# Kernel optimization log

Hardware: AMD Instinct MI355X
Metric: run time of the kernel (lower is better)

The kernel has to match this reference:

```python
import jax, jax.numpy as jnp
import numpy as np
import math

TAU = 2.0
V_TH = 1.0
DECAY = math.exp(-1.0 / TAU)  # LIF membrane decay


def setup_inputs() -> dict:
    key = jax.random.key(0)
    k_x, k_w, k_b = jax.random.split(key, 3)
    T, B, C_IN, H, W = 4, 8, 64, 128, 128
    C_OUT, K = 64, 3
    x = jax.random.normal(k_x, (T, B, C_IN, H, W), dtype=jnp.float32)
    fan_in = C_IN * K * K
    weight = jax.random.normal(k_w, (C_OUT, C_IN, K, K), dtype=jnp.float32) / jnp.sqrt(fan_in)
    bias = jax.random.normal(k_b, (C_OUT,), dtype=jnp.float32) * 0.01
    return {"x": x, "weight": weight, "bias": bias}


def reference(x, weight, bias):
    # x: [T, B, C_IN, H, W]; 3x3 conv, stride 1, pad 1 -> same spatial size
    T, B, C_IN, H, W = x.shape
    C_OUT = weight.shape[0]

    def conv(x_t):
        y = jax.lax.conv_general_dilated(
            x_t, weight,
            window_strides=(1, 1),
            padding=((1, 1), (1, 1)),
            dimension_numbers=("NCHW", "OIHW", "NCHW"),
        )
        return y + bias[None, :, None, None]

    def step(v, x_t):
        v_temp = v * DECAY + conv(x_t)            # membrane decay + synaptic input
        spike = (v_temp > V_TH).astype(v_temp.dtype)  # threshold fire
        v_next = v_temp * (1.0 - spike)           # soft reset
        return v_next, spike

    v0 = jnp.zeros((B, C_OUT, H, W), dtype=jnp.float32)
    _, spikes = jax.lax.scan(step, v0, x)         # spikes: [T, B, C_OUT, H, W]
    return spikes
```

## Files before the change

kernel.cpp:

```cpp
#include <hip/hip_runtime.h>

#define T_STEPS 4
#define BATCH   8
#define C_IN    64
#define C_OUT   64
#define HH      128
#define WW      128
#define TH      8
#define TW      16
#define ROWS    (TH + 2)
#define RLEN    24

#define DECAY_F32 0.6065306597126334f

__global__ void wt_build_kernel(const float* __restrict__ w, float* __restrict__ wt) {
    int tid = blockIdx.x * blockDim.x + threadIdx.x;
    if (tid >= 9 * C_IN * C_OUT) return;
    int co = tid & 63;
    int ci = (tid >> 6) & 63;
    int j  = tid >> 12;
    wt[tid] = w[(co * C_IN + ci) * 9 + j];
}

__global__ __launch_bounds__(512, 2) void snn_exact_kernel(
    const float* __restrict__ x,
    const float* __restrict__ wt,
    const float* __restrict__ bias,
    float* __restrict__ out)
{
    __shared__ __align__(16) float sx[C_IN][ROWS][RLEN];

    const int tid  = threadIdx.x;
    const int wid  = __builtin_amdgcn_readfirstlane(tid >> 6);
    const int lane = tid & 63;
    const int y    = lane & 3;
    const int xcol = lane >> 2;
    const int sy   = (wid >> 2) << 2;
    const int cob  = (wid & 3) << 4;
    const int b    = blockIdx.z;
    const int gy0  = blockIdx.y * TH;
    const int gx0  = blockIdx.x * TW;

    float bv[16];
#pragma unroll
    for (int o = 0; o < 16; ++o) bv[o] = bias[cob + o];

    float v[16];
#pragma unroll
    for (int o = 0; o < 16; ++o) v[o] = 0.0f;

    for (int t = 0; t < T_STEPS; ++t) {
        __syncthreads();
        const float* xsrc = x + ((size_t)(t * BATCH + b) * C_IN) * (HH * WW);
        for (int e = tid; e < C_IN * ROWS * 18; e += 512) {
            int ci  = e / (ROWS * 18);
            int rem = e - ci * (ROWS * 18);
            int row = rem / 18;
            int col = rem - row * 18;
            int gy  = gy0 + row - 1;
            int gx  = gx0 + col - 1;
            float val = 0.0f;
            if ((unsigned)gy < (unsigned)HH && (unsigned)gx < (unsigned)WW)
                val = xsrc[ci * (HH * WW) + gy * WW + gx];
            sx[ci][row][col] = val;
        }
        __syncthreads();

        float acc[16];
#pragma unroll
        for (int o = 0; o < 16; ++o) acc[o] = 0.0f;

#define TAP(KY, KX)                                                                   \
        {                                                                             \
            const float* wj = wt + ((KY) * 3 + (KX)) * (C_IN * C_OUT) + cob;          \
            _Pragma("unroll 4")                                                       \
            for (int ci = 0; ci < C_IN; ++ci) {                                       \
                const float xv = sx[ci][sy + y + (KY)][xcol + (KX)];                  \
                const float* wp = wj + (ci << 6);                                     \
                _Pragma("unroll")                                                     \
                for (int o = 0; o < 16; ++o)                                          \
                    acc[o] = fmaf(xv, wp[o], acc[o]);                                 \
            }                                                                         \
        }

        TAP(0, 0) TAP(0, 1) TAP(0, 2)
        TAP(1, 0) TAP(1, 1) TAP(1, 2)
        TAP(2, 0) TAP(2, 1) TAP(2, 2)
#undef TAP

        float* obase = out + ((size_t)(t * BATCH + b) * C_OUT + cob) * (HH * WW)
                     + (gy0 + sy + y) * WW + gx0 + xcol;
#pragma unroll
        for (int o = 0; o < 16; ++o) {
            float cb = __fadd_rn(acc[o], bv[o]);
            float vt = __fadd_rn(__fmul_rn(v[o], DECAY_F32), cb);
            bool fire = vt > 1.0f;
            v[o] = fire ? 0.0f : vt;
            obase[(size_t)o * (HH * WW)] = fire ? 1.0f : 0.0f;
        }
    }
}

extern "C" void kernel_launch(void* const* d_in, const int* in_sizes, int n_in,
                              void* d_out, int out_size, void* d_ws, size_t ws_size,
                              hipStream_t stream) {
    const float* x    = (const float*)d_in[0];
    const float* w    = (const float*)d_in[1];
    const float* bias = (const float*)d_in[2];
    float* out = (float*)d_out;
    float* wt  = (float*)d_ws;

    hipLaunchKernelGGL(wt_build_kernel, dim3((9 * C_IN * C_OUT + 255) / 256), dim3(256), 0, stream, w, wt);
    hipLaunchKernelGGL(snn_exact_kernel, dim3(WW / TW, HH / TH, BATCH), dim3(512), 0, stream,
                       x, wt, bias, out);
}
```

Baseline: 478.4 us.

## Store input tile channel-innermost in LDS and read four channels per float4

```diff
diff --git a/kernel.cpp b/kernel.cpp
--- a/kernel.cpp
+++ b/kernel.cpp
@@ -9,7 +9,8 @@
 #define TH      8
 #define TW      16
 #define ROWS    (TH + 2)
-#define RLEN    24
+#define COLS    18
+#define CPAD    68
 
 #define DECAY_F32 0.6065306597126334f
 
@@ -22,13 +23,13 @@
     wt[tid] = w[(co * C_IN + ci) * 9 + j];
 }
 
-__global__ __launch_bounds__(512, 2) void snn_exact_kernel(
+__global__ __launch_bounds__(512) void snn_exact_kernel(
     const float* __restrict__ x,
     const float* __restrict__ wt,
     const float* __restrict__ bias,
     float* __restrict__ out)
 {
-    __shared__ __align__(16) float sx[C_IN][ROWS][RLEN];
+    __shared__ __align__(16) float sx[ROWS * COLS * CPAD];
 
     const int tid  = threadIdx.x;
     const int wid  = __builtin_amdgcn_readfirstlane(tid >> 6);
@@ -41,9 +42,9 @@
     const int gy0  = blockIdx.y * TH;
     const int gx0  = blockIdx.x * TW;
 
-    float bv[16];
-#pragma unroll
-    for (int o = 0; o < 16; ++o) bv[o] = bias[cob + o];
+    const float* bp = bias + cob;
+
+    const float* xbase = &sx[((sy + y) * COLS + xcol) * CPAD];
 
     float v[16];
 #pragma unroll
@@ -52,17 +53,17 @@
     for (int t = 0; t < T_STEPS; ++t) {
         __syncthreads();
         const float* xsrc = x + ((size_t)(t * BATCH + b) * C_IN) * (HH * WW);
-        for (int e = tid; e < C_IN * ROWS * 18; e += 512) {
-            int ci  = e / (ROWS * 18);
-            int rem = e - ci * (ROWS * 18);
-            int row = rem / 18;
-            int col = rem - row * 18;
+        for (int e = tid; e < C_IN * ROWS * COLS; e += 512) {
+            int ci  = e / (ROWS * COLS);
+            int rem = e - ci * (ROWS * COLS);
+            int row = rem / COLS;
+            int col = rem - row * COLS;
             int gy  = gy0 + row - 1;
             int gx  = gx0 + col - 1;
             float val = 0.0f;
             if ((unsigned)gy < (unsigned)HH && (unsigned)gx < (unsigned)WW)
                 val = xsrc[ci * (HH * WW) + gy * WW + gx];
-            sx[ci][row][col] = val;
+            sx[(row * COLS + col) * CPAD + ci] = val;
         }
         __syncthreads();
 
@@ -73,13 +74,18 @@
 #define TAP(KY, KX)                                                                   \
         {                                                                             \
             const float* wj = wt + ((KY) * 3 + (KX)) * (C_IN * C_OUT) + cob;          \
-            _Pragma("unroll 4")                                                       \
-            for (int ci = 0; ci < C_IN; ++ci) {                                       \
-                const float xv = sx[ci][sy + y + (KY)][xcol + (KX)];                  \
-                const float* wp = wj + (ci << 6);                                     \
+            const float* xt = xbase + ((KY) * COLS + (KX)) * CPAD;                    \
+            _Pragma("unroll 2")                                                       \
+            for (int ci0 = 0; ci0 < C_IN; ci0 += 4) {                                 \
+                const float4 xv = *reinterpret_cast<const float4*>(xt + ci0);         \
+                const float xq[4] = {xv.x, xv.y, xv.z, xv.w};                         \
                 _Pragma("unroll")                                                     \
-                for (int o = 0; o < 16; ++o)                                          \
-                    acc[o] = fmaf(xv, wp[o], acc[o]);                                 \
+                for (int k = 0; k < 4; ++k) {                                         \
+                    const float* wp = wj + ((ci0 + k) << 6);                          \
+                    _Pragma("unroll")                                                 \
+                    for (int o = 0; o < 16; ++o)                                      \
+                        acc[o] = fmaf(xq[k], wp[o], acc[o]);                          \
+                }                                                                     \
             }                                                                         \
         }
 
@@ -92,7 +98,7 @@
                      + (gy0 + sy + y) * WW + gx0 + xcol;
 #pragma unroll
         for (int o = 0; o < 16; ++o) {
-            float cb = __fadd_rn(acc[o], bv[o]);
+            float cb = __fadd_rn(acc[o], bp[o]);
             float vt = __fadd_rn(__fmul_rn(v[o], DECAY_F32), cb);
             bool fire = vt > 1.0f;
             v[o] = fire ? 0.0f : vt;
```

After: 529.9 us. +10.8%, slower.
